# Kernel optimization log

Measured on AMD Instinct MI355X. Metric: run time of the kernel, lower is better.

## Reference

```python
import jax, jax.numpy as jnp
import numpy as np

N = 50000
E = 800000
G = 64
H, C = 16, 4  # heads, out_channels per head; H*C = 64


def setup_inputs() -> dict:
    key = jax.random.key(0)
    ks = jax.random.split(key, 16)
    return {
        "x": jax.random.normal(ks[0], (N,), jnp.float32),
        "edge_index": jax.random.randint(ks[1], (2, E), 0, N),
        "edge_attr": jax.random.normal(ks[2], (E,), jnp.float32),
        "batch": jnp.sort(jax.random.randint(ks[3], (N,), 0, G)),
        # GATv2Conv(1 -> 4, heads=16, edge_dim=1, concat=True)
        "Wl": jax.random.normal(ks[4], (1, H * C), jnp.float32) * 0.5,
        "bl": jnp.full((H * C,), 0.01, jnp.float32),
        "Wr": jax.random.normal(ks[5], (1, H * C), jnp.float32) * 0.5,
        "br": jnp.full((H * C,), 0.01, jnp.float32),
        "We": jax.random.normal(ks[6], (1, H * C), jnp.float32) * 0.5,
        "att": jax.random.normal(ks[7], (H, C), jnp.float32) * 0.5,
        "gat_bias": jnp.zeros((H * C,), jnp.float32),
        # GraphNorm(64)
        "gn_w": jnp.ones((H * C,), jnp.float32),
        "gn_b": jnp.zeros((H * C,), jnp.float32),
        "gn_ms": jnp.ones((H * C,), jnp.float32),
        # SAGEConv(64 -> 64, mean aggr, root weight)
        "sage_Wl": jax.random.normal(ks[8], (H * C, 64), jnp.float32) * 0.125,
        "sage_bl": jnp.full((64,), 0.01, jnp.float32),
        "sage_Wr": jax.random.normal(ks[9], (H * C, 64), jnp.float32) * 0.125,
        # MLP head
        "fc1_W": jax.random.normal(ks[10], (128, 2048), jnp.float32) * 0.08,
        "fc1_b": jnp.full((2048,), 0.01, jnp.float32),
        "fc2_W": jax.random.normal(ks[11], (2048, 1024), jnp.float32) * 0.02,
        "fc2_b": jnp.full((1024,), 0.01, jnp.float32),
        "fc3_W": jax.random.normal(ks[12], (1024, 3), jnp.float32) * 0.03,
        "fc3_b": jnp.full((3,), 0.01, jnp.float32),
    }


def reference(x, edge_index, edge_attr, batch, Wl, bl, Wr, br, We, att, gat_bias,
              gn_w, gn_b, gn_ms, sage_Wl, sage_bl, sage_Wr,
              fc1_W, fc1_b, fc2_W, fc2_b, fc3_W, fc3_b):
    src0, dst0 = edge_index[0], edge_index[1]
    x1 = x[:, None]  # [N,1] (torch.unsqueeze(x, -1))
    # ---- GATv2Conv ----
    xl = (x1 @ Wl + bl).reshape(N, H, C)  # source-side (x_j, also the value)
    xr = (x1 @ Wr + br).reshape(N, H, C)  # target-side (x_i)
    # add self loops; fill_value='mean' -> per-node mean of incoming edge_attr
    deg_in = jax.ops.segment_sum(jnp.ones((E,), x.dtype), dst0, num_segments=N)
    loop_attr = jax.ops.segment_sum(edge_attr, dst0, num_segments=N) / jnp.maximum(deg_in, 1.0)
    loops = jnp.arange(N)
    src = jnp.concatenate([src0, loops])
    dst = jnp.concatenate([dst0, loops])
    ea = jnp.concatenate([edge_attr, loop_attr])[:, None]  # [E+N,1]
    e = (ea @ We).reshape(-1, H, C)
    m = jax.nn.leaky_relu(xl[src] + xr[dst] + e, 0.2)  # [E+N,H,C]
    score = jnp.einsum('ehc,hc->eh', m, att)
    smax = jax.ops.segment_max(score, dst, num_segments=N)
    a = jnp.exp(score - smax[dst])
    denom = jax.ops.segment_sum(a, dst, num_segments=N)
    alpha = a / denom[dst]  # segmented softmax over incoming edges
    h = jax.ops.segment_sum(alpha[:, :, None] * xl[src], dst, num_segments=N)
    h = h.reshape(N, H * C) + gat_bias
    h = jax.nn.relu(h)
    # ---- GraphNorm ----
    cnt = jax.ops.segment_sum(jnp.ones((N,), x.dtype), batch, num_segments=G)[:, None]
    mean = jax.ops.segment_sum(h, batch, num_segments=G) / cnt
    o = h - mean[batch] * gn_ms
    var = jax.ops.segment_sum(o * o, batch, num_segments=G) / cnt
    h = gn_w * o / jnp.sqrt(var[batch] + 1e-5) + gn_b
    # ---- SAGEConv (mean aggregation + root weight) ----
    neigh = jax.ops.segment_sum(h[src0], dst0, num_segments=N) / jnp.maximum(deg_in, 1.0)[:, None]
    h = neigh @ sage_Wl + sage_bl + h @ sage_Wr
    h = jax.nn.relu(h)
    # ---- global max + mean pooling, MLP head (eval mode: dropout off) ----
    gmax = jax.ops.segment_max(h, batch, num_segments=G)
    gmean = jax.ops.segment_sum(h, batch, num_segments=G) / cnt
    g = jnp.concatenate([gmax, gmean], axis=1)  # [G, 128]
    g = jax.nn.relu(g @ fc1_W + fc1_b)
    g = jax.nn.relu(g @ fc2_W + fc2_b)
    return g @ fc3_W + fc3_b
```

## Files before the change

kernel.cpp:

```cpp
#include <hip/hip_runtime.h>

#define GG 64
#define HH 16
#define KK 64
#define S_SUB 8

__device__ __forceinline__ float bf2f(unsigned short u){
  return __uint_as_float(((unsigned)u) << 16);
}
__device__ __forceinline__ unsigned short f2bf(float f){
  unsigned u = __float_as_uint(f);
  unsigned r = u + 0x7fffu + ((u >> 16) & 1u);
  return (unsigned short)(r >> 16);
}


__global__ void k_count_rank(const int* __restrict__ ei, int* deg, int* __restrict__ rank, int E){
  int e = blockIdx.x*blockDim.x + threadIdx.x;
  if (e < E) rank[e] = atomicAdd(&deg[ei[E + e]], 1);
}

__global__ void k_scan1(const int* __restrict__ deg, int* __restrict__ bsum, int N){
  int base = blockIdx.x*1024;
  int lim = min(base + 1024, N);
  int s = 0;
  for (int i = base + (int)threadIdx.x; i < lim; i += 256) s += deg[i];
  #pragma unroll
  for (int ofs = 32; ofs >= 1; ofs >>= 1) s += __shfl_down(s, ofs, 64);
  __shared__ int ws[4];
  int lane = threadIdx.x & 63, wv = threadIdx.x >> 6;
  if (lane == 0) ws[wv] = s;
  __syncthreads();
  if (threadIdx.x == 0) bsum[blockIdx.x] = ws[0] + ws[1] + ws[2] + ws[3];
}

__global__ void __launch_bounds__(1024)
k_scan2(int* __restrict__ bsum, int* __restrict__ row_start_N, int NB){
  int t = threadIdx.x;
  int v = (t < NB) ? bsum[t] : 0;
  int lane = t & 63, wv = t >> 6;
  int val = v;
  #pragma unroll
  for (int ofs = 1; ofs < 64; ofs <<= 1){
    int tt = __shfl_up(val, ofs, 64);
    if (lane >= ofs) val += tt;
  }
  __shared__ int ws[16];
  if (lane == 63) ws[wv] = val;
  __syncthreads();
  if (t == 0){
    int run = 0;
    #pragma unroll
    for (int w = 0; w < 16; ++w){ int tmp = ws[w]; ws[w] = run; run += tmp; }
  }
  __syncthreads();
  int excl = ws[wv] + val - v;
  if (t < NB) bsum[t] = excl;
  if (t == NB - 1) *row_start_N = excl + v;
}

__global__ void k_scan3(const int* __restrict__ deg, const int* __restrict__ bsum,
                        int* __restrict__ row_start, int N){
  int b = blockIdx.x;
  int base = b*1024 + (int)threadIdx.x*4;
  int d0 = (base+0 < N) ? deg[base+0] : 0;
  int d1 = (base+1 < N) ? deg[base+1] : 0;
  int d2 = (base+2 < N) ? deg[base+2] : 0;
  int d3 = (base+3 < N) ? deg[base+3] : 0;
  int s = d0 + d1 + d2 + d3;
  int lane = threadIdx.x & 63, wv = threadIdx.x >> 6;
  int val = s;
  #pragma unroll
  for (int ofs = 1; ofs < 64; ofs <<= 1){
    int tt = __shfl_up(val, ofs, 64);
    if (lane >= ofs) val += tt;
  }
  __shared__ int ws[4];
  if (lane == 63) ws[wv] = val;
  __syncthreads();
  if (threadIdx.x == 0){
    int run = 0;
    #pragma unroll
    for (int w = 0; w < 4; ++w){ int tmp = ws[w]; ws[w] = run; run += tmp; }
  }
  __syncthreads();
  int pre = bsum[b] + ws[wv] + val - s;
  if (base+0 < N){ row_start[base+0] = pre; pre += d0; }
  if (base+1 < N){ row_start[base+1] = pre; pre += d1; }
  if (base+2 < N){ row_start[base+2] = pre; pre += d2; }
  if (base+3 < N){ row_start[base+3] = pre; }
}

__global__ void k_scatter(const int* __restrict__ ei, const float* __restrict__ ea,
                          const int* __restrict__ row_start, const int* __restrict__ rank,
                          int2* __restrict__ csr_se, int E){
  int e = blockIdx.x*blockDim.x + threadIdx.x;
  if (e >= E) return;
  int d = ei[E + e];
  int pos = row_start[d] + rank[e];
  csr_se[pos] = make_int2(ei[e], __float_as_int(ea[e]));
}

__global__ void k_gbounds(const int* __restrict__ batch, int N, int* __restrict__ goff){
  int g = threadIdx.x;
  if (g > GG) return;
  int lo = 0, hi = N;
  while (lo < hi){ int mid = (lo+hi) >> 1; if (batch[mid] < g) lo = mid+1; else hi = mid; }
  goff[g] = lo;
}

__global__ void k_gat(const float* __restrict__ x, const int* __restrict__ row_start,
                      const int2* __restrict__ cse,
                      const float* __restrict__ Wl, const float* __restrict__ bl,
                      const float* __restrict__ Wr, const float* __restrict__ br,
                      const float* __restrict__ We, const float* __restrict__ att,
                      const float* __restrict__ gat_bias,
                      float* __restrict__ h, int N){
  int t = blockIdx.x*blockDim.x + threadIdx.x;
  int n   = t >> 2;
  int sub = t & 3;
  if (n >= N) return;
  float xd = x[n];
  float wl[16], we[16], at[16], pre[16];
  int k0 = sub*16;
  #pragma unroll
  for (int i = 0; i < 16; ++i){
    int k = k0 + i;
    wl[i] = Wl[k]; we[i] = We[k]; at[i] = att[k];
    pre[i] = bl[k] + fmaf(xd, Wr[k], br[k]);
  }
  int e0 = row_start[n], e1 = row_start[n+1];
  float m[4]  = {-3.4e38f,-3.4e38f,-3.4e38f,-3.4e38f};
  float den[4] = {0,0,0,0}, S1[4] = {0,0,0,0};
  float asum = 0.f;

#define PROC(XS, EAV)                                                        \
  { float xs_ = (XS), ea_ = (EAV);                                           \
    _Pragma("unroll")                                                        \
    for (int hi2 = 0; hi2 < 4; ++hi2){                                       \
      float sc = 0.f;                                                        \
      _Pragma("unroll")                                                      \
      for (int c = 0; c < 4; ++c){                                           \
        int i = hi2*4 + c;                                                   \
        float tt = fmaf(xs_, wl[i], fmaf(ea_, we[i], pre[i]));               \
        tt = (tt > 0.f) ? tt : 0.2f*tt;                                      \
        sc = fmaf(tt, at[i], sc);                                            \
      }                                                                      \
      float nm = fmaxf(m[hi2], sc);                                          \
      float corr = __expf(m[hi2] - nm);                                      \
      float a    = __expf(sc - nm);                                          \
      den[hi2] = den[hi2]*corr + a;                                          \
      S1[hi2]  = S1[hi2] *corr + a*xs_;                                      \
      m[hi2] = nm; } }

  int e = e0;
  for (; e + 3 < e1; e += 4){
    int2 p0 = cse[e], p1 = cse[e+1], p2 = cse[e+2], p3 = cse[e+3];
    float xs0 = x[p0.x], xs1 = x[p1.x], xs2 = x[p2.x], xs3 = x[p3.x];
    float ea0 = __int_as_float(p0.y), ea1 = __int_as_float(p1.y);
    float ea2 = __int_as_float(p2.y), ea3 = __int_as_float(p3.y);
    asum += (ea0 + ea1) + (ea2 + ea3);
    PROC(xs0, ea0);
    PROC(xs1, ea1);
    PROC(xs2, ea2);
    PROC(xs3, ea3);
  }
  for (; e < e1; ++e){
    int2 p0 = cse[e];
    float xs0 = x[p0.x], ea0 = __int_as_float(p0.y);
    asum += ea0;
    PROC(xs0, ea0);
  }
  {
    float degf = (float)(e1 - e0);
    float eav = asum / fmaxf(degf, 1.0f);
    PROC(xd, eav);
  }
#undef PROC
  #pragma unroll
  for (int hi2 = 0; hi2 < 4; ++hi2){
    float r = S1[hi2] / den[hi2];
    float4 o;
    #pragma unroll
    for (int c = 0; c < 4; ++c){
      int i = hi2*4 + c, k = k0 + i;
      float v = fmaxf(fmaf(wl[i], r, bl[k] + gat_bias[k]), 0.f);
      ((float*)&o)[c] = v;
    }
    *(float4*)(h + (size_t)n*KK + k0 + hi2*4) = o;
  }
}

__global__ void k_gstats_part(const float* __restrict__ h, const int* __restrict__ goff,
                              float* __restrict__ gsum, float* __restrict__ gsum2){
  int g = blockIdx.x, sb = blockIdx.y;
  int s = goff[g], epos = goff[g+1];
  int k = threadIdx.x & 63, slice = threadIdx.x >> 6;
  float sum = 0.f, sum2 = 0.f;
  for (int n = s + sb*4 + slice; n < epos; n += S_SUB*4){
    float v = h[(size_t)n*KK + k];
    sum += v; sum2 += v*v;
  }
  __shared__ float ls[4][KK], ls2[4][KK];
  ls[slice][k] = sum; ls2[slice][k] = sum2;
  __syncthreads();
  if (slice == 0){
    float a  = ls[0][k]+ls[1][k]+ls[2][k]+ls[3][k];
    float b2 = ls2[0][k]+ls2[1][k]+ls2[2][k]+ls2[3][k];
    atomicAdd(&gsum[g*KK + k], a);
    atomicAdd(&gsum2[g*KK + k], b2);
  }
}

__global__ void k_norm(float* __restrict__ h, unsigned short* __restrict__ hb,
                       const int* __restrict__ batch,
                       const float* __restrict__ gsum, const float* __restrict__ gsum2,
                       const int* __restrict__ goff,
                       const float* __restrict__ gn_w, const float* __restrict__ gn_b,
                       const float* __restrict__ gn_ms, int N){
  int t = blockIdx.x*blockDim.x + threadIdx.x;
  if (t >= N*16) return;
  int n = t >> 4, q = t & 15;
  int b = batch[n];
  float c = fmaxf((float)(goff[b+1] - goff[b]), 1.0f);
  float inv = 1.0f / c;
  float4 hv = *(float4*)(h + (size_t)n*KK + q*4);
  float ov[4];
  #pragma unroll
  for (int i = 0; i < 4; ++i){
    int k = q*4 + i;
    float mean = gsum[b*KK + k]*inv;
    float eh2  = gsum2[b*KK + k]*inv;
    float ms = gn_ms[k];
    float var = eh2 - 2.f*ms*mean*mean + ms*ms*mean*mean;
    float sc = gn_w[k] * __frsqrt_rn(var + 1e-5f);
    float sh = gn_b[k] - sc*mean*ms;
    ov[i] = fmaf(sc, ((float*)&hv)[i], sh);
  }
  *(float4*)(h + (size_t)n*KK + q*4) = make_float4(ov[0], ov[1], ov[2], ov[3]);
  ushort4 bv;
  bv.x = f2bf(ov[0]); bv.y = f2bf(ov[1]); bv.z = f2bf(ov[2]); bv.w = f2bf(ov[3]);
  *(ushort4*)(hb + (size_t)n*KK + q*4) = bv;
}

__global__ void k_sage(const float* __restrict__ h, const unsigned short* __restrict__ hb,
                       const int* __restrict__ row_start, const int2* __restrict__ cse,
                       const float* __restrict__ Wl, const float* __restrict__ bln,
                       const float* __restrict__ Wr,
                       float* __restrict__ h2, int N){
  __shared__ float snm[16][KK], shn[16][KK];
  const ushort4* hb4 = (const ushort4*)hb;
  int tid = threadIdx.x;
  int u = tid >> 4;
  int q = tid & 15;
  int n = blockIdx.x*16 + u;
  if (n < N){
    int e0 = row_start[n], e1 = row_start[n+1];
    float a0=0.f,a1=0.f,a2=0.f,a3=0.f;
    float b0=0.f,b1=0.f,b2=0.f,b3=0.f;
    int e = e0;
    for (; e + 7 < e1; e += 8){
      int s0 = cse[e].x,   s1 = cse[e+1].x, s2 = cse[e+2].x, s3 = cse[e+3].x;
      int s4 = cse[e+4].x, s5 = cse[e+5].x, s6 = cse[e+6].x, s7 = cse[e+7].x;
      ushort4 v0 = hb4[(size_t)s0*16 + q];
      ushort4 v1 = hb4[(size_t)s1*16 + q];
      ushort4 v2 = hb4[(size_t)s2*16 + q];
      ushort4 v3 = hb4[(size_t)s3*16 + q];
      ushort4 v4 = hb4[(size_t)s4*16 + q];
      ushort4 v5 = hb4[(size_t)s5*16 + q];
      ushort4 v6 = hb4[(size_t)s6*16 + q];
      ushort4 v7 = hb4[(size_t)s7*16 + q];
      a0 += bf2f(v0.x); a1 += bf2f(v0.y); a2 += bf2f(v0.z); a3 += bf2f(v0.w);
      b0 += bf2f(v1.x); b1 += bf2f(v1.y); b2 += bf2f(v1.z); b3 += bf2f(v1.w);
      a0 += bf2f(v2.x); a1 += bf2f(v2.y); a2 += bf2f(v2.z); a3 += bf2f(v2.w);
      b0 += bf2f(v3.x); b1 += bf2f(v3.y); b2 += bf2f(v3.z); b3 += bf2f(v3.w);
      a0 += bf2f(v4.x); a1 += bf2f(v4.y); a2 += bf2f(v4.z); a3 += bf2f(v4.w);
      b0 += bf2f(v5.x); b1 += bf2f(v5.y); b2 += bf2f(v5.z); b3 += bf2f(v5.w);
      a0 += bf2f(v6.x); a1 += bf2f(v6.y); a2 += bf2f(v6.z); a3 += bf2f(v6.w);
      b0 += bf2f(v7.x); b1 += bf2f(v7.y); b2 += bf2f(v7.z); b3 += bf2f(v7.w);
    }
    for (; e < e1; ++e){
      ushort4 v0 = hb4[(size_t)cse[e].x*16 + q];
      a0 += bf2f(v0.x); a1 += bf2f(v0.y); a2 += bf2f(v0.z); a3 += bf2f(v0.w);
    }
    float dg = fmaxf((float)(e1 - e0), 1.0f);
    float inv = 1.0f/dg;
    float4 nm = make_float4((a0+b0)*inv, (a1+b1)*inv, (a2+b2)*inv, (a3+b3)*inv);
    *(float4*)&snm[u][q*4] = nm;
    *(float4*)&shn[u][q*4] = *(const float4*)(h + (size_t)n*KK + q*4);
  }
  __syncthreads();
  int j = tid & 63, u0 = tid >> 6;
  float acc[4];
  #pragma unroll
  for (int p = 0; p < 4; ++p) acc[p] = bln[j];
  for (int k = 0; k < KK; ++k){
    float wlv = Wl[k*KK + j], wrv = Wr[k*KK + j];
    #pragma unroll
    for (int p = 0; p < 4; ++p){
      int un = u0 + p*4;
      acc[p] = fmaf(snm[un][k], wlv, acc[p]);
      acc[p] = fmaf(shn[un][k], wrv, acc[p]);
    }
  }
  #pragma unroll
  for (int p = 0; p < 4; ++p){
    int un = u0 + p*4;
    int nn = blockIdx.x*16 + un;
    if (nn < N) h2[(size_t)nn*KK + j] = fmaxf(acc[p], 0.f);
  }
}

__global__ void k_pool_part(const float* __restrict__ h2, const int* __restrict__ goff,
                            unsigned* __restrict__ gmaxu, float* __restrict__ gsumP){
  int g = blockIdx.x, sb = blockIdx.y;
  int s = goff[g], epos = goff[g+1];
  int k = threadIdx.x & 63, slice = threadIdx.x >> 6;
  float mx = 0.f, sm = 0.f;
  for (int n = s + sb*4 + slice; n < epos; n += S_SUB*4){
    float v = h2[(size_t)n*KK + k];
    mx = fmaxf(mx, v); sm += v;
  }
  __shared__ float lm[4][KK], lsum[4][KK];
  lm[slice][k] = mx; lsum[slice][k] = sm;
  __syncthreads();
  if (slice == 0){
    float m2 = fmaxf(fmaxf(lm[0][k], lm[1][k]), fmaxf(lm[2][k], lm[3][k]));
    float s2 = lsum[0][k]+lsum[1][k]+lsum[2][k]+lsum[3][k];
    atomicMax(&gmaxu[g*KK + k], __float_as_uint(m2));
    atomicAdd(&gsumP[g*KK + k], s2);
  }
}


__global__ void k_fc1(const unsigned* __restrict__ gmaxu, const float* __restrict__ gsumP,
                      const int* __restrict__ goff,
                      const float* __restrict__ W, const float* __restrict__ b,
                      float* __restrict__ out){
  __shared__ float sin[128];
  int g = blockIdx.y, jt = blockIdx.x;
  int tid = threadIdx.x;
  if (tid < 128){
    float c = fmaxf((float)(goff[g+1] - goff[g]), 1.0f);
    sin[tid] = (tid < 64) ? __uint_as_float(gmaxu[g*64 + tid])
                          : gsumP[g*64 + (tid-64)] / c;
  }
  __syncthreads();
  int j = jt*256 + tid;
  float acc = b[j];
  #pragma unroll 16
  for (int k = 0; k < 128; ++k)
    acc = fmaf(sin[k], W[(size_t)k*2048 + j], acc);
  out[(size_t)g*2048 + j] = fmaxf(acc, 0.f);
}

__global__ void k_fc2a(const float* __restrict__ in, const float* __restrict__ W,
                       float* __restrict__ partial){
  __shared__ float sin[64][128];
  int jt = blockIdx.x, ks = blockIdx.y;
  int k0 = ks*128;
  int tid = threadIdx.x;
  for (int idx = tid; idx < 64*128; idx += 256){
    int g = idx >> 7, k = idx & 127;
    sin[g][k] = in[(size_t)g*2048 + k0 + k];
  }
  __syncthreads();
  int j = tid & 63, gs = tid >> 6;
  const float* Wp = W + (size_t)k0*1024 + jt*64 + j;
  float acc[16];
  #pragma unroll
  for (int p = 0; p < 16; ++p) acc[p] = 0.f;
  for (int k = 0; k < 128; ++k){
    float w = Wp[(size_t)k*1024];
    #pragma unroll
    for (int p = 0; p < 16; ++p)
      acc[p] = fmaf(sin[gs*16 + p][k], w, acc[p]);
  }
  #pragma unroll
  for (int p = 0; p < 16; ++p){
    int g = gs*16 + p;
    partial[((size_t)ks*64 + g)*1024 + jt*64 + j] = acc[p];
  }
}

__global__ void k_fc2red(const float* __restrict__ partial, const float* __restrict__ b,
                         float* __restrict__ out){
  int i = blockIdx.x*blockDim.x + threadIdx.x;
  int g = i >> 10, j = i & 1023;
  float s = b[j];
  #pragma unroll
  for (int ks = 0; ks < 16; ++ks)
    s += partial[((size_t)ks*64 + g)*1024 + j];
  out[i] = fmaxf(s, 0.f);
}

__global__ void k_fc3(const float* __restrict__ in, const float* __restrict__ W,
                      const float* __restrict__ b, float* __restrict__ out, int nOut){
  int w = (blockIdx.x*blockDim.x + threadIdx.x) >> 6;
  int lane = threadIdx.x & 63;
  if (w >= GG*nOut) return;
  int g = w / nOut, j = w - g*nOut;
  const float* row = in + (size_t)g*1024;
  float acc = 0.f;
  #pragma unroll
  for (int k = lane; k < 1024; k += 64)
    acc = fmaf(row[k], W[(size_t)k*nOut + j], acc);
  #pragma unroll
  for (int ofs = 32; ofs >= 1; ofs >>= 1)
    acc += __shfl_down(acc, ofs, 64);
  if (lane == 0) out[w] = acc + b[j];
}

extern "C" void kernel_launch(void* const* d_in, const int* in_sizes, int n_in,
                              void* d_out, int out_size, void* d_ws, size_t ws_size,
                              hipStream_t stream) {
  const float* x        = (const float*)d_in[0];
  const int*   ei       = (const int*)d_in[1];
  const float* ea       = (const float*)d_in[2];
  const int*   batch    = (const int*)d_in[3];
  const float* Wl       = (const float*)d_in[4];
  const float* bl       = (const float*)d_in[5];
  const float* Wr       = (const float*)d_in[6];
  const float* br       = (const float*)d_in[7];
  const float* We       = (const float*)d_in[8];
  const float* att      = (const float*)d_in[9];
  const float* gat_bias = (const float*)d_in[10];
  const float* gn_w     = (const float*)d_in[11];
  const float* gn_b     = (const float*)d_in[12];
  const float* gn_ms    = (const float*)d_in[13];
  const float* sage_Wl  = (const float*)d_in[14];
  const float* sage_bl  = (const float*)d_in[15];
  const float* sage_Wr  = (const float*)d_in[16];
  const float* fc1_W    = (const float*)d_in[17];
  const float* fc1_b    = (const float*)d_in[18];
  const float* fc2_W    = (const float*)d_in[19];
  const float* fc2_b    = (const float*)d_in[20];
  const float* fc3_W    = (const float*)d_in[21];
  const float* fc3_b    = (const float*)d_in[22];

  const int N = in_sizes[0];
  const int E = in_sizes[1] / 2;
  const int NB = (N + 1023) / 1024;

  char* ws = (char*)d_ws;
  size_t off = 0;
  auto alloc = [&](size_t bytes){ void* p = ws + off; off += (bytes + 255) & ~(size_t)255; return p; };

  int*      deg_i  = (int*)alloc((size_t)N*4);
  float*    gsum   = (float*)alloc(GG*KK*4);
  float*    gsum2  = (float*)alloc(GG*KK*4);
  unsigned* gmaxu  = (unsigned*)alloc(GG*KK*4);
  float*    gsumP  = (float*)alloc(GG*KK*4);
  size_t zero_bytes = off;
  int*   rank      = (int*)alloc((size_t)E*4);
  int*   bsum      = (int*)alloc((size_t)NB*4);
  int*   row_start = (int*)alloc((size_t)(N+1)*4);
  int*   goff      = (int*)alloc((GG+1)*4);
  int2*  csr_se    = (int2*)alloc((size_t)E*8);
  float* h         = (float*)alloc((size_t)N*KK*4);
  unsigned short* hb = (unsigned short*)alloc((size_t)N*KK*2);
  float* h2        = (float*)alloc((size_t)N*KK*4);
  float* out1      = (float*)alloc((size_t)GG*2048*4);
  float* out2      = (float*)alloc((size_t)GG*1024*4);
  float* partial   = (float*)alloc((size_t)16*GG*1024*4);
  (void)ws_size; (void)n_in; (void)out_size;

  hipMemsetAsync(d_ws, 0, zero_bytes, stream);

  const int B = 256;
  k_count_rank<<<(E+B-1)/B, B, 0, stream>>>(ei, deg_i, rank, E);
  k_gbounds<<<1, 128, 0, stream>>>(batch, N, goff);
  k_scan1  <<<NB, B, 0, stream>>>(deg_i, bsum, N);
  k_scan2  <<<1, 1024, 0, stream>>>(bsum, row_start + N, NB);
  k_scan3  <<<NB, B, 0, stream>>>(deg_i, bsum, row_start, N);
  k_scatter<<<(E+B-1)/B, B, 0, stream>>>(ei, ea, row_start, rank, csr_se, E);
  k_gat    <<<((size_t)N*4+B-1)/B, B, 0, stream>>>(x, row_start, csr_se,
                                                   Wl, bl, Wr, br, We, att, gat_bias, h, N);
  {
    dim3 grid(GG, S_SUB);
    k_gstats_part<<<grid, 256, 0, stream>>>(h, goff, gsum, gsum2);
  }
  k_norm   <<<((size_t)N*16+B-1)/B, B, 0, stream>>>(h, hb, batch, gsum, gsum2, goff,
                                                    gn_w, gn_b, gn_ms, N);
  k_sage   <<<(N+15)/16, B, 0, stream>>>(h, hb, row_start, csr_se, sage_Wl, sage_bl, sage_Wr, h2, N);
  {
    dim3 grid(GG, S_SUB);
    k_pool_part<<<grid, 256, 0, stream>>>(h2, goff, gmaxu, gsumP);
  }
  {
    dim3 grid(8, GG);
    k_fc1  <<<grid, 256, 0, stream>>>(gmaxu, gsumP, goff, fc1_W, fc1_b, out1);
  }
  {
    dim3 grid(16, 16);
    k_fc2a <<<grid, 256, 0, stream>>>(out1, fc2_W, partial);
  }
  k_fc2red <<<(GG*1024+B-1)/B, B, 0, stream>>>(partial, fc2_b, out2);
  k_fc3    <<<(GG*3*64+B-1)/B, B, 0, stream>>>(out2, fc3_W, fc3_b, (float*)d_out, 3);
}
```

Measured before the change: 207.3 us.

## Fuse workspace zeroing with group bounds and use nontemporal CSR accesses

```diff
diff --git a/kernel.cpp b/kernel.cpp
--- a/kernel.cpp
+++ b/kernel.cpp
@@ -12,6 +12,29 @@
   unsigned u = __float_as_uint(f);
   unsigned r = u + 0x7fffu + ((u >> 16) & 1u);
   return (unsigned short)(r >> 16);
+}
+
+__device__ __forceinline__ void nt_store_i2(int2 v, int2* p){
+  long long w = ((unsigned long long)(unsigned)v.y << 32) | (unsigned)v.x;
+  __builtin_nontemporal_store(w, (long long*)p);
+}
+__device__ __forceinline__ int2 nt_load_i2(const int2* p){
+  long long w = __builtin_nontemporal_load((const long long*)p);
+  int2 r; r.x = (int)(unsigned)(w & 0xffffffffu); r.y = (int)(unsigned)(w >> 32);
+  return r;
+}
+
+__global__ void k_zero(int4* __restrict__ p, int nInt4,
+                       const int* __restrict__ batch, int N, int* __restrict__ goff){
+  int t = blockIdx.x*blockDim.x + threadIdx.x;
+  for (int i = t; i < nInt4; i += gridDim.x*blockDim.x)
+    p[i] = make_int4(0,0,0,0);
+  if (blockIdx.x == 0 && threadIdx.x <= GG){
+    int g = threadIdx.x;
+    int lo = 0, hi = N;
+    while (lo < hi){ int mid = (lo+hi) >> 1; if (batch[mid] < g) lo = mid+1; else hi = mid; }
+    goff[g] = lo;
+  }
 }
 
 
@@ -98,15 +121,7 @@
   if (e >= E) return;
   int d = ei[E + e];
   int pos = row_start[d] + rank[e];
-  csr_se[pos] = make_int2(ei[e], __float_as_int(ea[e]));
-}
-
-__global__ void k_gbounds(const int* __restrict__ batch, int N, int* __restrict__ goff){
-  int g = threadIdx.x;
-  if (g > GG) return;
-  int lo = 0, hi = N;
-  while (lo < hi){ int mid = (lo+hi) >> 1; if (batch[mid] < g) lo = mid+1; else hi = mid; }
-  goff[g] = lo;
+  nt_store_i2(make_int2(ei[e], __float_as_int(ea[e])), &csr_se[pos]);
 }
 
 __global__ void k_gat(const float* __restrict__ x, const int* __restrict__ row_start,
@@ -155,7 +170,10 @@
 
   int e = e0;
   for (; e + 3 < e1; e += 4){
-    int2 p0 = cse[e], p1 = cse[e+1], p2 = cse[e+2], p3 = cse[e+3];
+    int2 p0 = nt_load_i2(&cse[e]);
+    int2 p1 = nt_load_i2(&cse[e+1]);
+    int2 p2 = nt_load_i2(&cse[e+2]);
+    int2 p3 = nt_load_i2(&cse[e+3]);
     float xs0 = x[p0.x], xs1 = x[p1.x], xs2 = x[p2.x], xs3 = x[p3.x];
     float ea0 = __int_as_float(p0.y), ea1 = __int_as_float(p1.y);
     float ea2 = __int_as_float(p2.y), ea3 = __int_as_float(p3.y);
@@ -260,8 +278,14 @@
     float b0=0.f,b1=0.f,b2=0.f,b3=0.f;
     int e = e0;
     for (; e + 7 < e1; e += 8){
-      int s0 = cse[e].x,   s1 = cse[e+1].x, s2 = cse[e+2].x, s3 = cse[e+3].x;
-      int s4 = cse[e+4].x, s5 = cse[e+5].x, s6 = cse[e+6].x, s7 = cse[e+7].x;
+      int s0 = nt_load_i2(&cse[e]).x;
+      int s1 = nt_load_i2(&cse[e+1]).x;
+      int s2 = nt_load_i2(&cse[e+2]).x;
+      int s3 = nt_load_i2(&cse[e+3]).x;
+      int s4 = nt_load_i2(&cse[e+4]).x;
+      int s5 = nt_load_i2(&cse[e+5]).x;
+      int s6 = nt_load_i2(&cse[e+6]).x;
+      int s7 = nt_load_i2(&cse[e+7]).x;
       ushort4 v0 = hb4[(size_t)s0*16 + q];
       ushort4 v1 = hb4[(size_t)s1*16 + q];
       ushort4 v2 = hb4[(size_t)s2*16 + q];
@@ -465,11 +489,13 @@
   float* partial   = (float*)alloc((size_t)16*GG*1024*4);
   (void)ws_size; (void)n_in; (void)out_size;
 
-  hipMemsetAsync(d_ws, 0, zero_bytes, stream);
-
   const int B = 256;
+  {
+    int nInt4 = (int)(zero_bytes >> 4);
+    int blocks = min((nInt4 + B - 1)/B, 256);
+    k_zero <<<blocks, B, 0, stream>>>((int4*)d_ws, nInt4, batch, N, goff);
+  }
   k_count_rank<<<(E+B-1)/B, B, 0, stream>>>(ei, deg_i, rank, E);
-  k_gbounds<<<1, 128, 0, stream>>>(batch, N, goff);
   k_scan1  <<<NB, B, 0, stream>>>(deg_i, bsum, N);
   k_scan2  <<<1, 1024, 0, stream>>>(bsum, row_start + N, NB);
   k_scan3  <<<NB, B, 0, stream>>>(deg_i, bsum, row_start, N);
```

Measured after the change: 225.9 us. 1.09x slower.
